# Kernel tuning notes

Measured on AMD Instinct MI355X. Metric: run time of the kernel, lower is better.

## Reference

```python
import jax, jax.numpy as jnp
import numpy as np

NUM_HEADS = 8
DIM = 64
DEPTH = DIM // NUM_HEADS  # 8
F = 64  # input feature dim


def setup_inputs() -> dict:
    key = jax.random.key(0)
    ks = jax.random.split(key, 5)
    x = jax.random.normal(ks[0], (4, 2048, F), dtype=jnp.float32)
    # per-head weights stacked: [H, F, depth]; initializer 'normal' ~ N(0, 0.05) in keras,
    # but scale does not change the math structure; use small normal.
    Wq = jax.random.normal(ks[1], (NUM_HEADS, F, DEPTH), dtype=jnp.float32) * 0.05
    Wk = jax.random.normal(ks[2], (NUM_HEADS, F, DEPTH), dtype=jnp.float32) * 0.05
    Wv = jax.random.normal(ks[3], (NUM_HEADS, F, DEPTH), dtype=jnp.float32) * 0.05
    Wo = jax.random.normal(ks[4], (NUM_HEADS * DEPTH, F), dtype=jnp.float32) * 0.05
    return {"x": x, "Wq": Wq, "Wk": Wk, "Wv": Wv, "Wo": Wo}


def reference(x, Wq, Wk, Wv, Wo):
    # x: [B, S, F]; Wq/Wk/Wv: [H, F, D]; Wo: [H*D, F]
    q = jnp.einsum("bsf,hfd->hbsd", x, Wq)
    k = jnp.einsum("bsf,hfd->hbsd", x, Wk)
    v = jnp.einsum("bsf,hfd->hbsd", x, Wv)
    scores = jnp.einsum("hbsd,hbtd->hbst", q, k) / jnp.sqrt(jnp.float32(DEPTH))
    weights = jax.nn.softmax(scores, axis=-1)  # [H, B, S, S]
    heads = jnp.einsum("hbst,hbtd->hbsd", weights, v)  # [H, B, S, D]
    # concat heads along last dim -> [B, S, H*D]
    B, S = x.shape[0], x.shape[1]
    concat = jnp.transpose(heads, (1, 2, 0, 3)).reshape(B, S, NUM_HEADS * DEPTH)
    out = concat @ Wo  # [B, S, F]
    # return_sequences=False -> sum over sequence axis
    return jnp.sum(out, axis=1), weights
```

## Files before the change

### kernel.cpp

```cpp
#include <hip/hip_runtime.h>
#include <cstdint>
#include <cstddef>

#define NH 8
#define NB 4
#define SS 2048
#define FF 64
#define DD 8
#define QKV_SZ (NH*NB*SS*DD)

__device__ __forceinline__ float wave_sum64(float x) {
#define DPP_STEP(ctrl, rm) { int t_ = __builtin_amdgcn_update_dpp(0, __float_as_int(x), (ctrl), (rm), 0xf, true); x += __int_as_float(t_); }
  DPP_STEP(0x111, 0xf)
  DPP_STEP(0x112, 0xf)
  DPP_STEP(0x114, 0xf)
  DPP_STEP(0x118, 0xf)
  DPP_STEP(0x142, 0xa)
  DPP_STEP(0x143, 0xc)
#undef DPP_STEP
  return x;
}

__global__ __launch_bounds__(256) void qkv_kernel(
    const float* __restrict__ x,
    const float* __restrict__ Wq, const float* __restrict__ Wk, const float* __restrict__ Wv,
    float* __restrict__ Qo, float* __restrict__ Ko, float* __restrict__ Vo) {
  __shared__ float xT[64][64];
  const int tid = threadIdx.x;
  const int row0 = blockIdx.x * 64;
  #pragma unroll
  for (int k = 0; k < 4; ++k) {
    int flat4 = tid + 256 * k;
    int r = flat4 >> 4, fq = flat4 & 15;
    float4 xv = reinterpret_cast<const float4*>(x)[(size_t)(row0 + r) * 16 + fq];
    xT[fq * 4 + 0][r] = xv.x; xT[fq * 4 + 1][r] = xv.y;
    xT[fq * 4 + 2][r] = xv.z; xT[fq * 4 + 3][r] = xv.w;
  }
  __syncthreads();
  const int r = tid & 63;
  const int g = __builtin_amdgcn_readfirstlane(tid >> 6);
  const int obase = g * 48;
  float acc[48];
  #pragma unroll
  for (int i = 0; i < 48; ++i) acc[i] = 0.f;
  for (int f = 0; f < 64; ++f) {
    float xv = xT[f][r];
    #pragma unroll
    for (int i = 0; i < 48; ++i) {
      int o = obase + i;
      const float* Wsel = (o < 64) ? Wq : ((o < 128) ? Wk : Wv);
      int oc = o & 63;
      acc[i] = fmaf(xv, Wsel[((oc >> 3) << 9) + f * 8 + (oc & 7)], acc[i]);
    }
  }
  const int row = row0 + r;
  const int b = row >> 11, s = row & 2047;
  const float qscale = 0.35355339059327373f;
  #pragma unroll
  for (int i = 0; i < 48; ++i) {
    int o = obase + i;
    int m = o >> 6, oc = o & 63, h = oc >> 3, d = oc & 7;
    float v = acc[i];
    if (m == 0) v *= qscale;
    float* dst = (m == 0) ? Qo : ((m == 1) ? Ko : Vo);
    dst[(((size_t)(h * NB + b) * SS) + s) * DD + d] = v;
  }
}

__global__ __launch_bounds__(256, 4) void attn_kernel(
    const float* __restrict__ Qg, const float* __restrict__ Kg, const float* __restrict__ Vg,
    float* __restrict__ wOut, float* __restrict__ hsum2) {
  __shared__ float psum[64][9];
  __shared__ float rinv_s[64];
  __shared__ float hred[4][8];
  const int tid = threadIdx.x;
  const int lane = tid & 63;
  const int w = tid >> 6;
  const int bx = blockIdx.x;
  const int hb = bx >> 5;
  const int rt = bx & 31;
  const int r0 = rt * 64;
  const float* Kbase = Kg + (size_t)hb * SS * DD;
  const float* Vbase = Vg + (size_t)hb * SS * DD;
  const float4* Qv = reinterpret_cast<const float4*>(Qg + (size_t)hb * SS * DD + (size_t)r0 * DD);
  float* wBase = wOut + (size_t)hb * SS * SS + (size_t)r0 * SS;

  for (int ci = 0; ci < 2; ++ci) {
    const int c = w * 2 + ci;
    const int tbase = c * 256;
    float Kf[4][8];
    #pragma unroll
    for (int j = 0; j < 4; ++j) {
      const float4* kp = reinterpret_cast<const float4*>(Kbase + (size_t)(tbase + 64 * j + lane) * DD);
      float4 a = kp[0], bv = kp[1];
      Kf[j][0] = a.x;  Kf[j][1] = a.y;  Kf[j][2] = a.z;  Kf[j][3] = a.w;
      Kf[j][4] = bv.x; Kf[j][5] = bv.y; Kf[j][6] = bv.z; Kf[j][7] = bv.w;
    }
    float4 qa = Qv[0], qb = Qv[1];
    for (int r = 0; r < 64; ++r) {
      int rn = (r < 63) ? (r + 1) : 63;
      float4 na = Qv[rn * 2], nb = Qv[rn * 2 + 1];
      float q[8] = {qa.x, qa.y, qa.z, qa.w, qb.x, qb.y, qb.z, qb.w};
      float part = 0.f;
      #pragma unroll
      for (int j = 0; j < 4; ++j) {
        float sc = 0.f;
        #pragma unroll
        for (int d = 0; d < 8; ++d) sc = fmaf(q[d], Kf[j][d], sc);
        part += __expf(sc);
      }
      float tot = wave_sum64(part);
      if (lane == 63) psum[r][c] = tot;
      qa = na; qb = nb;
    }
  }
  __syncthreads();
  if (tid < 64) {
    float ssum = 0.f;
    #pragma unroll
    for (int k = 0; k < 8; ++k) ssum += psum[tid][k];
    rinv_s[tid] = 1.0f / ssum;
  }
  __syncthreads();

  float A[8] = {0.f, 0.f, 0.f, 0.f, 0.f, 0.f, 0.f, 0.f};
  for (int ci = 0; ci < 4; ++ci) {
    const int c = w * 4 + ci;
    const int tbase = c * 128;
    float Kf[2][8], Vf[2][8];
    #pragma unroll
    for (int j = 0; j < 2; ++j) {
      const float4* kp = reinterpret_cast<const float4*>(Kbase + (size_t)(tbase + 64 * j + lane) * DD);
      float4 a = kp[0], bv = kp[1];
      Kf[j][0] = a.x;  Kf[j][1] = a.y;  Kf[j][2] = a.z;  Kf[j][3] = a.w;
      Kf[j][4] = bv.x; Kf[j][5] = bv.y; Kf[j][6] = bv.z; Kf[j][7] = bv.w;
      const float4* vp = reinterpret_cast<const float4*>(Vbase + (size_t)(tbase + 64 * j + lane) * DD);
      float4 va = vp[0], vb = vp[1];
      Vf[j][0] = va.x; Vf[j][1] = va.y; Vf[j][2] = va.z; Vf[j][3] = va.w;
      Vf[j][4] = vb.x; Vf[j][5] = vb.y; Vf[j][6] = vb.z; Vf[j][7] = vb.w;
    }
    float4 qa = Qv[0], qb = Qv[1];
    for (int r = 0; r < 64; ++r) {
      int rn = (r < 63) ? (r + 1) : 63;
      float4 na = Qv[rn * 2], nb = Qv[rn * 2 + 1];
      float q[8] = {qa.x, qa.y, qa.z, qa.w, qb.x, qb.y, qb.z, qb.w};
      float rin = rinv_s[r];
      float p[2];
      #pragma unroll
      for (int j = 0; j < 2; ++j) {
        float sc = 0.f;
        #pragma unroll
        for (int d = 0; d < 8; ++d) sc = fmaf(q[d], Kf[j][d], sc);
        p[j] = __expf(sc) * rin;
      }
      float* wr = wBase + (size_t)r * SS + tbase + lane;
      wr[0] = p[0];
      wr[64] = p[1];
      #pragma unroll
      for (int j = 0; j < 2; ++j)
        #pragma unroll
        for (int d = 0; d < 8; ++d) A[d] = fmaf(p[j], Vf[j][d], A[d]);
      qa = na; qb = nb;
    }
  }

  #pragma unroll
  for (int d = 0; d < 8; ++d) {
    float t = wave_sum64(A[d]);
    if (lane == 63) hred[w][d] = t;
  }
  __syncthreads();
  if (tid < 8) {
    float t = hred[0][tid] + hred[1][tid] + hred[2][tid] + hred[3][tid];
    hsum2[(size_t)bx * 8 + tid] = t;
  }
}

__global__ __launch_bounds__(256) void out_kernel(
    const float* __restrict__ hsum2, const float* __restrict__ Wo,
    float* __restrict__ out) {
  __shared__ float ch[256];
  const int tid = threadIdx.x;
  {
    int hb = tid >> 3, d = tid & 7;
    float s = 0.f;
    for (int rtile = 0; rtile < 32; ++rtile) s += hsum2[(size_t)(hb * 32 + rtile) * 8 + d];
    ch[tid] = s;
  }
  __syncthreads();
  const int b = tid >> 6, f = tid & 63;
  float acc = 0.f;
  for (int h = 0; h < 8; ++h) {
    #pragma unroll
    for (int d = 0; d < 8; ++d) {
      acc = fmaf(ch[(h * 4 + b) * 8 + d], Wo[(h * 8 + d) * 64 + f], acc);
    }
  }
  out[b * 64 + f] = acc;
}

extern "C" void kernel_launch(void* const* d_in, const int* in_sizes, int n_in,
                              void* d_out, int out_size, void* d_ws, size_t ws_size,
                              hipStream_t stream) {
  const float* x  = (const float*)d_in[0];
  const float* Wq = (const float*)d_in[1];
  const float* Wk = (const float*)d_in[2];
  const float* Wv = (const float*)d_in[3];
  const float* Wo = (const float*)d_in[4];
  float* out = (float*)d_out;
  float* wts = out + 256;
  float* ws = (float*)d_ws;
  float* Q = ws;
  float* K = ws + QKV_SZ;
  float* V = ws + 2 * (size_t)QKV_SZ;
  float* hs = ws + 3 * (size_t)QKV_SZ;

  qkv_kernel<<<128, 256, 0, stream>>>(x, Wq, Wk, Wv, Q, K, V);
  attn_kernel<<<1024, 256, 0, stream>>>(Q, K, V, wts, hs);
  out_kernel<<<1, 256, 0, stream>>>(hs, Wo, out);
}
```

Baseline: 672.8 us.

## Restructure attention softmax pass, column-sum V product, and split QKV grid

The QKV projection now runs on a 2D grid with half the outputs per thread, and its LDS tile is padded to avoid bank conflicts. In attention, the row-sum pass assigns one query row per lane and reads K tiles from LDS, which removes the per-row wave reductions. The second pass writes float2 weights and accumulates per-key column sums of probabilities, so the V multiply happens once per key instead of once per row. This exploits the final sum over the sequence and cuts the FMA work. Q is cached in LDS, at the cost of more shared memory per block.

Result: faster. 613.8 us (-8.8%).

```diff
diff --git a/kernel.cpp b/kernel.cpp
--- a/kernel.cpp
+++ b/kernel.cpp
@@ -25,7 +25,7 @@
     const float* __restrict__ x,
     const float* __restrict__ Wq, const float* __restrict__ Wk, const float* __restrict__ Wv,
     float* __restrict__ Qo, float* __restrict__ Ko, float* __restrict__ Vo) {
-  __shared__ float xT[64][64];
+  __shared__ float xT[64][65];
   const int tid = threadIdx.x;
   const int row0 = blockIdx.x * 64;
   #pragma unroll
@@ -39,14 +39,14 @@
   __syncthreads();
   const int r = tid & 63;
   const int g = __builtin_amdgcn_readfirstlane(tid >> 6);
-  const int obase = g * 48;
-  float acc[48];
-  #pragma unroll
-  for (int i = 0; i < 48; ++i) acc[i] = 0.f;
+  const int obase = g * 24 + blockIdx.y * 96;
+  float acc[24];
+  #pragma unroll
+  for (int i = 0; i < 24; ++i) acc[i] = 0.f;
   for (int f = 0; f < 64; ++f) {
     float xv = xT[f][r];
     #pragma unroll
-    for (int i = 0; i < 48; ++i) {
+    for (int i = 0; i < 24; ++i) {
       int o = obase + i;
       const float* Wsel = (o < 64) ? Wq : ((o < 128) ? Wk : Wv);
       int oc = o & 63;
@@ -57,7 +57,7 @@
   const int b = row >> 11, s = row & 2047;
   const float qscale = 0.35355339059327373f;
   #pragma unroll
-  for (int i = 0; i < 48; ++i) {
+  for (int i = 0; i < 24; ++i) {
     int o = obase + i;
     int m = o >> 6, oc = o & 63, h = oc >> 3, d = oc & 7;
     float v = acc[i];
@@ -70,7 +70,9 @@
 __global__ __launch_bounds__(256, 4) void attn_kernel(
     const float* __restrict__ Qg, const float* __restrict__ Kg, const float* __restrict__ Vg,
     float* __restrict__ wOut, float* __restrict__ hsum2) {
-  __shared__ float psum[64][9];
+  __shared__ float4 klds[4 * 512];
+  __shared__ float4 qlds[128];
+  __shared__ float psum[4][64];
   __shared__ float rinv_s[64];
   __shared__ float hred[4][8];
   const int tid = threadIdx.x;
@@ -82,86 +84,82 @@
   const int r0 = rt * 64;
   const float* Kbase = Kg + (size_t)hb * SS * DD;
   const float* Vbase = Vg + (size_t)hb * SS * DD;
-  const float4* Qv = reinterpret_cast<const float4*>(Qg + (size_t)hb * SS * DD + (size_t)r0 * DD);
+  const float4* K4 = reinterpret_cast<const float4*>(Kbase);
+  const float4* Q4 = reinterpret_cast<const float4*>(Qg + (size_t)hb * SS * DD + (size_t)r0 * DD);
   float* wBase = wOut + (size_t)hb * SS * SS + (size_t)r0 * SS;
 
-  for (int ci = 0; ci < 2; ++ci) {
-    const int c = w * 2 + ci;
-    const int tbase = c * 256;
-    float Kf[4][8];
+  if (tid < 128) qlds[tid] = Q4[tid];
+
+  float4 qa = Q4[lane * 2], qb = Q4[lane * 2 + 1];
+  const float q0 = qa.x, q1 = qa.y, q2 = qa.z, q3 = qa.w;
+  const float q4_ = qb.x, q5 = qb.y, q6 = qb.z, q7 = qb.w;
+  float rs0 = 0.f, rs1 = 0.f;
+  float4* kw = klds + w * 512;
+  for (int cc = 0; cc < 2; ++cc) {
+    const int t0 = (w * 2 + cc) * 256;
     #pragma unroll
-    for (int j = 0; j < 4; ++j) {
-      const float4* kp = reinterpret_cast<const float4*>(Kbase + (size_t)(tbase + 64 * j + lane) * DD);
-      float4 a = kp[0], bv = kp[1];
-      Kf[j][0] = a.x;  Kf[j][1] = a.y;  Kf[j][2] = a.z;  Kf[j][3] = a.w;
-      Kf[j][4] = bv.x; Kf[j][5] = bv.y; Kf[j][6] = bv.z; Kf[j][7] = bv.w;
-    }
-    float4 qa = Qv[0], qb = Qv[1];
-    for (int r = 0; r < 64; ++r) {
-      int rn = (r < 63) ? (r + 1) : 63;
-      float4 na = Qv[rn * 2], nb = Qv[rn * 2 + 1];
-      float q[8] = {qa.x, qa.y, qa.z, qa.w, qb.x, qb.y, qb.z, qb.w};
-      float part = 0.f;
-      #pragma unroll
-      for (int j = 0; j < 4; ++j) {
-        float sc = 0.f;
-        #pragma unroll
-        for (int d = 0; d < 8; ++d) sc = fmaf(q[d], Kf[j][d], sc);
-        part += __expf(sc);
-      }
-      float tot = wave_sum64(part);
-      if (lane == 63) psum[r][c] = tot;
-      qa = na; qb = nb;
-    }
-  }
-  __syncthreads();
-  if (tid < 64) {
-    float ssum = 0.f;
-    #pragma unroll
-    for (int k = 0; k < 8; ++k) ssum += psum[tid][k];
-    rinv_s[tid] = 1.0f / ssum;
-  }
+    for (int i = 0; i < 8; ++i) kw[lane + 64 * i] = K4[(size_t)t0 * 2 + lane + 64 * i];
+    float4 a0 = kw[0], b0 = kw[1], a1 = kw[2], b1 = kw[3];
+    #pragma unroll 2
+    for (int tt = 0; tt < 256; tt += 2) {
+      const int tn = (tt + 2 < 256) ? (tt + 2) : 254;
+      float4 na0 = kw[2 * tn], nb0 = kw[2 * tn + 1];
+      float4 na1 = kw[2 * tn + 2], nb1 = kw[2 * tn + 3];
+      float s0 = q0 * a0.x;
+      s0 = fmaf(q1, a0.y, s0); s0 = fmaf(q2, a0.z, s0); s0 = fmaf(q3, a0.w, s0);
+      s0 = fmaf(q4_, b0.x, s0); s0 = fmaf(q5, b0.y, s0); s0 = fmaf(q6, b0.z, s0);
+      s0 = fmaf(q7, b0.w, s0);
+      float s1 = q0 * a1.x;
+      s1 = fmaf(q1, a1.y, s1); s1 = fmaf(q2, a1.z, s1); s1 = fmaf(q3, a1.w, s1);
+      s1 = fmaf(q4_, b1.x, s1); s1 = fmaf(q5, b1.y, s1); s1 = fmaf(q6, b1.z, s1);
+      s1 = fmaf(q7, b1.w, s1);
+      rs0 += __expf(s0);
+      rs1 += __expf(s1);
+      a0 = na0; b0 = nb0; a1 = na1; b1 = nb1;
+    }
+  }
+  psum[w][lane] = rs0 + rs1;
+  __syncthreads();
+  if (tid < 64)
+    rinv_s[tid] = 1.0f / (psum[0][tid] + psum[1][tid] + psum[2][tid] + psum[3][tid]);
   __syncthreads();
 
   float A[8] = {0.f, 0.f, 0.f, 0.f, 0.f, 0.f, 0.f, 0.f};
   for (int ci = 0; ci < 4; ++ci) {
     const int c = w * 4 + ci;
     const int tbase = c * 128;
-    float Kf[2][8], Vf[2][8];
-    #pragma unroll
-    for (int j = 0; j < 2; ++j) {
-      const float4* kp = reinterpret_cast<const float4*>(Kbase + (size_t)(tbase + 64 * j + lane) * DD);
-      float4 a = kp[0], bv = kp[1];
-      Kf[j][0] = a.x;  Kf[j][1] = a.y;  Kf[j][2] = a.z;  Kf[j][3] = a.w;
-      Kf[j][4] = bv.x; Kf[j][5] = bv.y; Kf[j][6] = bv.z; Kf[j][7] = bv.w;
-      const float4* vp = reinterpret_cast<const float4*>(Vbase + (size_t)(tbase + 64 * j + lane) * DD);
-      float4 va = vp[0], vb = vp[1];
-      Vf[j][0] = va.x; Vf[j][1] = va.y; Vf[j][2] = va.z; Vf[j][3] = va.w;
-      Vf[j][4] = vb.x; Vf[j][5] = vb.y; Vf[j][6] = vb.z; Vf[j][7] = vb.w;
-    }
-    float4 qa = Qv[0], qb = Qv[1];
+    const float4* kp = reinterpret_cast<const float4*>(Kbase + (size_t)(tbase + 2 * lane) * DD);
+    float4 k0a = kp[0], k0b = kp[1], k1a = kp[2], k1b = kp[3];
+    float4 qa2 = qlds[0], qb2 = qlds[1];
+    float cs0 = 0.f, cs1 = 0.f;
     for (int r = 0; r < 64; ++r) {
-      int rn = (r < 63) ? (r + 1) : 63;
-      float4 na = Qv[rn * 2], nb = Qv[rn * 2 + 1];
-      float q[8] = {qa.x, qa.y, qa.z, qa.w, qb.x, qb.y, qb.z, qb.w};
-      float rin = rinv_s[r];
-      float p[2];
-      #pragma unroll
-      for (int j = 0; j < 2; ++j) {
-        float sc = 0.f;
-        #pragma unroll
-        for (int d = 0; d < 8; ++d) sc = fmaf(q[d], Kf[j][d], sc);
-        p[j] = __expf(sc) * rin;
-      }
-      float* wr = wBase + (size_t)r * SS + tbase + lane;
-      wr[0] = p[0];
-      wr[64] = p[1];
-      #pragma unroll
-      for (int j = 0; j < 2; ++j)
-        #pragma unroll
-        for (int d = 0; d < 8; ++d) A[d] = fmaf(p[j], Vf[j][d], A[d]);
-      qa = na; qb = nb;
-    }
+      const int rn = (r < 63) ? (r + 1) : 63;
+      float4 na = qlds[rn * 2], nb = qlds[rn * 2 + 1];
+      const float rin = rinv_s[r];
+      float s0 = qa2.x * k0a.x;
+      s0 = fmaf(qa2.y, k0a.y, s0); s0 = fmaf(qa2.z, k0a.z, s0); s0 = fmaf(qa2.w, k0a.w, s0);
+      s0 = fmaf(qb2.x, k0b.x, s0); s0 = fmaf(qb2.y, k0b.y, s0); s0 = fmaf(qb2.z, k0b.z, s0);
+      s0 = fmaf(qb2.w, k0b.w, s0);
+      float s1 = qa2.x * k1a.x;
+      s1 = fmaf(qa2.y, k1a.y, s1); s1 = fmaf(qa2.z, k1a.z, s1); s1 = fmaf(qa2.w, k1a.w, s1);
+      s1 = fmaf(qb2.x, k1b.x, s1); s1 = fmaf(qb2.y, k1b.y, s1); s1 = fmaf(qb2.z, k1b.z, s1);
+      s1 = fmaf(qb2.w, k1b.w, s1);
+      float p0 = __expf(s0) * rin;
+      float p1 = __expf(s1) * rin;
+      reinterpret_cast<float2*>(wBase + (size_t)r * SS + tbase)[lane] = make_float2(p0, p1);
+      cs0 += p0; cs1 += p1;
+      qa2 = na; qb2 = nb;
+    }
+    const float4* vp = reinterpret_cast<const float4*>(Vbase + (size_t)(tbase + 2 * lane) * DD);
+    float4 v0a = vp[0], v0b = vp[1], v1a = vp[2], v1b = vp[3];
+    A[0] = fmaf(cs0, v0a.x, A[0]); A[0] = fmaf(cs1, v1a.x, A[0]);
+    A[1] = fmaf(cs0, v0a.y, A[1]); A[1] = fmaf(cs1, v1a.y, A[1]);
+    A[2] = fmaf(cs0, v0a.z, A[2]); A[2] = fmaf(cs1, v1a.z, A[2]);
+    A[3] = fmaf(cs0, v0a.w, A[3]); A[3] = fmaf(cs1, v1a.w, A[3]);
+    A[4] = fmaf(cs0, v0b.x, A[4]); A[4] = fmaf(cs1, v1b.x, A[4]);
+    A[5] = fmaf(cs0, v0b.y, A[5]); A[5] = fmaf(cs1, v1b.y, A[5]);
+    A[6] = fmaf(cs0, v0b.z, A[6]); A[6] = fmaf(cs1, v1b.z, A[6]);
+    A[7] = fmaf(cs0, v0b.w, A[7]); A[7] = fmaf(cs1, v1b.w, A[7]);
   }
 
   #pragma unroll
@@ -215,7 +213,7 @@
   float* V = ws + 2 * (size_t)QKV_SZ;
   float* hs = ws + 3 * (size_t)QKV_SZ;
 
-  qkv_kernel<<<128, 256, 0, stream>>>(x, Wq, Wk, Wv, Q, K, V);
+  qkv_kernel<<<dim3(128, 2), 256, 0, stream>>>(x, Wq, Wk, Wv, Q, K, V);
   attn_kernel<<<1024, 256, 0, stream>>>(Q, K, V, wts, hs);
   out_kernel<<<1, 256, 0, stream>>>(hs, Wo, out);
 }
```
